# Kernel optimization log

Hardware: AMD Instinct MI355X
Metric: run time of the kernel (lower is better)

## Reference

```python
import math
import jax, jax.numpy as jnp
import numpy as np

B, K_LEN, Q_LEN = 16, 1024, 1024
E, N_HEAD, H = 1024, 8, 128

def setup_inputs() -> dict:
    key = jax.random.key(0)
    ks = jax.random.split(key, 7)
    k = jax.random.normal(ks[0], (B, K_LEN, E), dtype=jnp.float32)
    q = jax.random.normal(ks[1], (B, Q_LEN, E), dtype=jnp.float32)
    w_kx = jax.random.normal(ks[2], (N_HEAD, E, H), dtype=jnp.float32) * (1.0 / math.sqrt(E))
    w_qx = jax.random.normal(ks[3], (N_HEAD, E, H), dtype=jnp.float32) * (1.0 / math.sqrt(E))
    proj_w = jax.random.normal(ks[4], (E, N_HEAD * H), dtype=jnp.float32) * (1.0 / math.sqrt(N_HEAD * H))
    proj_b = jax.random.normal(ks[5], (E,), dtype=jnp.float32) * 0.01
    memory_len = jax.random.randint(ks[6], (B,), 0, K_LEN, dtype=jnp.int32)
    return {"k": k, "q": q, "w_kx": w_kx, "w_qx": w_qx, "proj_w": proj_w, "proj_b": proj_b, "memory_len": memory_len}

def reference(k, q, w_kx, w_qx, proj_w, proj_b, memory_len):
    n_head, embed_dim, hidden = w_kx.shape
    mb, k_len, _ = k.shape
    q_len = q.shape[1]
    # Faithful replication of torch repeat/view pairing:
    # row idx in [0, n_head*mb): data batch = idx % mb, weight head = idx % n_head
    idx = jnp.arange(n_head * mb)
    kx = jnp.einsum('nse,neh->nsh', k[idx % mb], w_kx[idx % n_head])   # [nB, k_len, H]
    qx = jnp.einsum('nse,neh->nsh', q[idx % mb], w_qx[idx % n_head])   # [nB, q_len, H]
    score = jnp.einsum('nqh,nkh->nqk', qx, kx) / math.sqrt(hidden)     # [nB, q_len, k_len]
    # 1D memory_len path: per-batch key-length mask, tiled over heads
    valid = jnp.arange(k_len)[None, :] < memory_len[:, None]           # [B, k_len]
    valid = jnp.tile(valid, (n_head, 1))[:, None, :]                   # [nB, 1, k_len]
    score = jnp.where(valid, score, jnp.float32(-10000.0))
    attn = jax.nn.softmax(score, axis=-1)
    out = jnp.einsum('nqk,nkh->nqh', attn, kx)                         # [nB, q_len, H]
    # torch.cat(torch.split(out, mb, 0), -1): chunk j -> feature block j
    out = out.reshape(n_head, mb, q_len, hidden).transpose(1, 2, 0, 3).reshape(mb, q_len, n_head * hidden)
    out = out @ proj_w.T + proj_b                                      # [B, q_len, E]
    return out, attn
```

## Files before the change

### kernel.cpp

```cpp
#include <hip/hip_runtime.h>
#include <hip/hip_bf16.h>

#define NBATCH 16
#define SEQ    1024
#define EDIM   1024
#define HDIM   128
#define RSQRT_H 0.08838834764831845f


typedef short s8b __attribute__((ext_vector_type(8)));
typedef float f32x4 __attribute__((ext_vector_type(4)));

__device__ __forceinline__ unsigned short bfr(float f) {
    unsigned u = __float_as_uint(f);
    u += 0x7fffu + ((u >> 16) & 1u);
    return (unsigned short)(u >> 16);
}

__device__ __forceinline__ f32x4 MFMA(s8b a, s8b b, f32x4 c) {
    return __builtin_amdgcn_mfma_f32_16x16x32_bf16(a, b, c, 0, 0, 0);
}

__global__ __launch_bounds__(256) void projx_mfma(const float* __restrict__ X,
                                                  const unsigned short* __restrict__ WT,
                                                  unsigned short* __restrict__ OUT) {
    const int b  = blockIdx.y;
    const int bm = blockIdx.x * 32;
    const int lane = threadIdx.x & 63, w = threadIdx.x >> 6;
    const int wn = w * 32;
    const int r = lane & 15, ko4 = lane >> 4, ko = ko4 * 8;

    const unsigned short* Bb = WT + (size_t)(b & 7) * 131072 + (size_t)(wn + r) * 1024 + ko;
    const float* Ab = X + (size_t)b * 1048576 + (size_t)(bm + r) * 1024 + ko;
    f32x4 acc[2][2] = {};

    for (int k = 0; k < 1024; k += 32) {
        s8b a0, a1;
        float4 u0 = *(const float4*)(Ab + k);
        float4 u1 = *(const float4*)(Ab + k + 4);
        a0[0]=(short)bfr(u0.x); a0[1]=(short)bfr(u0.y);
        a0[2]=(short)bfr(u0.z); a0[3]=(short)bfr(u0.w);
        a0[4]=(short)bfr(u1.x); a0[5]=(short)bfr(u1.y);
        a0[6]=(short)bfr(u1.z); a0[7]=(short)bfr(u1.w);
        float4 v0 = *(const float4*)(Ab + (size_t)16 * 1024 + k);
        float4 v1 = *(const float4*)(Ab + (size_t)16 * 1024 + k + 4);
        a1[0]=(short)bfr(v0.x); a1[1]=(short)bfr(v0.y);
        a1[2]=(short)bfr(v0.z); a1[3]=(short)bfr(v0.w);
        a1[4]=(short)bfr(v1.x); a1[5]=(short)bfr(v1.y);
        a1[6]=(short)bfr(v1.z); a1[7]=(short)bfr(v1.w);
        s8b b0 = *(const s8b*)(Bb + k);
        s8b b1 = *(const s8b*)(Bb + (size_t)16 * 1024 + k);
        acc[0][0] = MFMA(a0, b0, acc[0][0]);
        acc[0][1] = MFMA(a0, b1, acc[0][1]);
        acc[1][0] = MFMA(a1, b0, acc[1][0]);
        acc[1][1] = MFMA(a1, b1, acc[1][1]);
    }
#pragma unroll
    for (int i = 0; i < 2; ++i)
#pragma unroll
    for (int j = 0; j < 2; ++j) {
        const int row0 = bm + i * 16 + ko4 * 4;
        const int col  = wn + j * 16 + r;
#pragma unroll
        for (int jj = 0; jj < 4; ++jj)
            OUT[((size_t)b * SEQ + row0 + jj) * HDIM + col] = bfr(acc[i][j][jj]);
    }
}

__global__ __launch_bounds__(256) void projout_mfma(const float* __restrict__ Ap,
                                                    const unsigned short* __restrict__ Bp,
                                                    float* __restrict__ Cp,
                                                    const float* __restrict__ bias) {
    const int b  = blockIdx.z;
    const int bm = blockIdx.x * 64, bn = blockIdx.y * 64;
    const int lane = threadIdx.x & 63, w = threadIdx.x >> 6;
    const int wm = (w >> 1) * 32, wn = (w & 1) * 32;
    const int r = lane & 15, ko4 = lane >> 4, ko = ko4 * 8;

    const unsigned short* Bb = Bp + (size_t)(bn + wn + r) * HDIM + ko;
    const float* Ab = (const float*)Ap + (size_t)b * SEQ * HDIM
                      + (size_t)(bm + wm + r) * HDIM + ko;
    f32x4 acc[2][2] = {};
    for (int k = 0; k < HDIM; k += 32) {
        s8b a0, a1;
        float4 u0 = *(const float4*)(Ab + k);
        float4 u1 = *(const float4*)(Ab + k + 4);
        a0[0]=(short)bfr(u0.x); a0[1]=(short)bfr(u0.y);
        a0[2]=(short)bfr(u0.z); a0[3]=(short)bfr(u0.w);
        a0[4]=(short)bfr(u1.x); a0[5]=(short)bfr(u1.y);
        a0[6]=(short)bfr(u1.z); a0[7]=(short)bfr(u1.w);
        float4 v0 = *(const float4*)(Ab + (size_t)16 * HDIM + k);
        float4 v1 = *(const float4*)(Ab + (size_t)16 * HDIM + k + 4);
        a1[0]=(short)bfr(v0.x); a1[1]=(short)bfr(v0.y);
        a1[2]=(short)bfr(v0.z); a1[3]=(short)bfr(v0.w);
        a1[4]=(short)bfr(v1.x); a1[5]=(short)bfr(v1.y);
        a1[6]=(short)bfr(v1.z); a1[7]=(short)bfr(v1.w);
        s8b b0 = *(const s8b*)(Bb + k);
        s8b b1 = *(const s8b*)(Bb + (size_t)16 * HDIM + k);
        acc[0][0] = MFMA(a0, b0, acc[0][0]);
        acc[0][1] = MFMA(a0, b1, acc[0][1]);
        acc[1][0] = MFMA(a1, b0, acc[1][0]);
        acc[1][1] = MFMA(a1, b1, acc[1][1]);
    }
#pragma unroll
    for (int i = 0; i < 2; ++i)
#pragma unroll
    for (int j = 0; j < 2; ++j) {
        const int row0 = bm + wm + i * 16 + ko4 * 4;
        const int col  = bn + wn + j * 16 + r;
        const float bv = bias[col];
#pragma unroll
        for (int jj = 0; jj < 4; ++jj)
            Cp[(size_t)b * SEQ * EDIM + (size_t)(row0 + jj) * EDIM + col]
                = acc[i][j][jj] + bv;
    }
}

__global__ __launch_bounds__(256) void weff_kernel(const float* __restrict__ proj_w,
                                                   unsigned short* __restrict__ weffb) {
    int i = blockIdx.x * 256 + threadIdx.x;
    int e = i >> 7, h = i & 127;
    const float* p = proj_w + (size_t)e * (8 * HDIM) + h;
    float s = 0.f;
#pragma unroll
    for (int j = 0; j < 8; ++j) s += p[j * HDIM];
    weffb[i] = bfr(s);
}

__global__ __launch_bounds__(256) void wt_kernel(const float* __restrict__ src,
                                                 unsigned short* __restrict__ dst) {
    __shared__ unsigned short tile[32][40];
    const int hd = blockIdx.z, e0 = blockIdx.x * 32, h0 = blockIdx.y * 32;
    const int t = threadIdx.x, r = t >> 3, c = (t & 7) * 4;
    float4 v = *(const float4*)(src + ((size_t)hd * 1024 + e0 + r) * 128 + h0 + c);
    tile[r][c]     = bfr(v.x);
    tile[r][c + 1] = bfr(v.y);
    tile[r][c + 2] = bfr(v.z);
    tile[r][c + 3] = bfr(v.w);
    __syncthreads();
    ushort4 o;
    o.x = tile[c][r]; o.y = tile[c + 1][r]; o.z = tile[c + 2][r]; o.w = tile[c + 3][r];
    *(ushort4*)(dst + ((size_t)hd * 128 + h0 + r) * 1024 + e0 + c) = o;
}

__global__ __launch_bounds__(256) void kxt_kernel(const unsigned short* __restrict__ src,
                                                  unsigned short* __restrict__ dst) {
    __shared__ unsigned short tile[32][40];
    const int b = blockIdx.z, s0 = blockIdx.x * 32, h0 = blockIdx.y * 32;
    const int t = threadIdx.x, r = t >> 3, c = (t & 7) * 4;
    *(ushort4*)&tile[r][c] =
        *(const ushort4*)(src + ((size_t)b * 1024 + s0 + r) * 128 + h0 + c);
    __syncthreads();
    ushort4 o;
    o.x = tile[c][r]; o.y = tile[c + 1][r]; o.z = tile[c + 2][r]; o.w = tile[c + 3][r];
    *(ushort4*)(dst + ((size_t)b * 128 + h0 + r) * 1024 + s0 + c) = o;
}

__global__ __launch_bounds__(256) void fused_attn(
        const unsigned short* __restrict__ qxh, const unsigned short* __restrict__ kxh,
        const unsigned short* __restrict__ kxT, const int* __restrict__ mlen,
        float* __restrict__ attn0, float* __restrict__ outb) {
    __shared__ unsigned short Ph[16][1048];
    __shared__ float redm[4][16];
    __shared__ float redl[4][16];

    const int flat = blockIdx.y * 64 + blockIdx.x;
    const int work = (flat & 7) * 128 + (flat >> 3);
    const int b  = work >> 6;
    const int q0 = (work & 63) * 16;

    const int t = threadIdx.x, w = t >> 6, lane = t & 63;
    const int r = lane & 15, ko4 = lane >> 4, ko = ko4 * 8;
    const int ml = mlen[b];

    s8b aq[4];
#pragma unroll
    for (int ks = 0; ks < 4; ++ks)
        aq[ks] = *(const s8b*)(qxh + ((size_t)b * SEQ + q0 + r) * HDIM + ks * 32 + ko);

    f32x4 sacc[16];
#pragma unroll
    for (int i = 0; i < 16; ++i) {
        const int n0 = (w + 4 * i) * 16;
        f32x4 acc = {};
#pragma unroll
        for (int ks = 0; ks < 4; ++ks) {
            s8b bk = *(const s8b*)(kxh + ((size_t)b * SEQ + n0 + r) * HDIM + ks * 32 + ko);
            acc = MFMA(aq[ks], bk, acc);
        }
        sacc[i] = acc;
    }

    float pm[4] = {-3.0e38f, -3.0e38f, -3.0e38f, -3.0e38f};
#pragma unroll
    for (int i = 0; i < 16; ++i) {
        const int col = (w + 4 * i) * 16 + r;
#pragma unroll
        for (int jj = 0; jj < 4; ++jj) {
            float x = sacc[i][jj] * RSQRT_H;
            x = (col < ml) ? x : -10000.0f;
            sacc[i][jj] = x;
            pm[jj] = fmaxf(pm[jj], x);
        }
    }
#pragma unroll
    for (int d = 1; d < 16; d <<= 1)
#pragma unroll
        for (int jj = 0; jj < 4; ++jj) pm[jj] = fmaxf(pm[jj], __shfl_xor(pm[jj], d));
    if (r == 0) {
#pragma unroll
        for (int jj = 0; jj < 4; ++jj) redm[w][ko4 * 4 + jj] = pm[jj];
    }
    __syncthreads();
    float m[4];
#pragma unroll
    for (int jj = 0; jj < 4; ++jj) {
        const int row = ko4 * 4 + jj;
        m[jj] = fmaxf(fmaxf(redm[0][row], redm[1][row]),
                      fmaxf(redm[2][row], redm[3][row]));
    }
    float pl[4] = {0.f, 0.f, 0.f, 0.f};
#pragma unroll
    for (int i = 0; i < 16; ++i)
#pragma unroll
        for (int jj = 0; jj < 4; ++jj) {
            float e = __expf(sacc[i][jj] - m[jj]);
            sacc[i][jj] = e;
            pl[jj] += e;
        }
#pragma unroll
    for (int d = 1; d < 16; d <<= 1)
#pragma unroll
        for (int jj = 0; jj < 4; ++jj) pl[jj] += __shfl_xor(pl[jj], d);
    if (r == 0) {
#pragma unroll
        for (int jj = 0; jj < 4; ++jj) redl[w][ko4 * 4 + jj] = pl[jj];
    }
    __syncthreads();
    float li[4];
#pragma unroll
    for (int jj = 0; jj < 4; ++jj) {
        const int row = ko4 * 4 + jj;
        li[jj] = 1.0f / (redl[0][row] + redl[1][row] + redl[2][row] + redl[3][row]);
    }

    const size_t RB = (size_t)NBATCH * SEQ * SEQ;
    float* base0 = attn0 + (size_t)b * SEQ * SEQ;
    const bool wr2 = (b >= 7);
#pragma unroll
    for (int i = 0; i < 16; ++i) {
        const int n0 = (w + 4 * i) * 16;
#pragma unroll
        for (int jj = 0; jj < 4; ++jj) {
            const int row = ko4 * 4 + jj;
            const float y = sacc[i][jj] * li[jj];
            const size_t off = (size_t)(q0 + row) * SEQ + n0 + r;
            base0[off]          = y;
            base0[off + RB]     = y;
            base0[off + 3 * RB] = y;
            base0[off + 4 * RB] = y;
            base0[off + 5 * RB] = y;
            base0[off + 6 * RB] = y;
            base0[off + 7 * RB] = y;
            if (wr2) base0[off + 2 * RB] = y;
            Ph[row][n0 + r] = bfr(y);
        }
    }
    __syncthreads();

    f32x4 acc2[2] = {};
    for (int ks = 0; ks < 32; ++ks) {
        s8b pa = *(const s8b*)(&Ph[r][ks * 32 + ko]);
#pragma unroll
        for (int c = 0; c < 2; ++c) {
            const int n0 = (w * 2 + c) * 16;
            s8b bk = *(const s8b*)(kxT + ((size_t)b * HDIM + n0 + r) * SEQ + ks * 32 + ko);
            acc2[c] = MFMA(pa, bk, acc2[c]);
        }
    }
#pragma unroll
    for (int c = 0; c < 2; ++c) {
        const int n0 = (w * 2 + c) * 16;
#pragma unroll
        for (int jj = 0; jj < 4; ++jj)
            outb[((size_t)b * SEQ + q0 + ko4 * 4 + jj) * HDIM + n0 + r] = acc2[c][jj];
    }
}

__global__ __launch_bounds__(256) void fixup_kernel(const uint4* __restrict__ src,
                                                    uint4* __restrict__ dst) {
    size_t i = (size_t)blockIdx.x * 256 + threadIdx.x;
    dst[i] = src[i];
}

extern "C" void kernel_launch(void* const* d_in, const int* in_sizes, int n_in,
                              void* d_out, int out_size, void* d_ws, size_t ws_size,
                              hipStream_t stream) {
    const float* k      = (const float*)d_in[0];
    const float* q      = (const float*)d_in[1];
    const float* w_kx   = (const float*)d_in[2];
    const float* w_qx   = (const float*)d_in[3];
    const float* proj_w = (const float*)d_in[4];
    const float* proj_b = (const float*)d_in[5];
    const int*   mlen   = (const int*)d_in[6];

    float* out0  = (float*)d_out;
    float* attn0 = out0 + (size_t)NBATCH * SEQ * EDIM;
    const size_t BLK = (size_t)NBATCH * SEQ * SEQ;

    unsigned short* sc16 = (unsigned short*)(attn0 + 2 * BLK);
    unsigned short* wkT   = sc16;
    unsigned short* wqT   = wkT + 1048576;
    unsigned short* weffb = wqT + 1048576;
    unsigned short* qxh   = weffb + 131072;
    unsigned short* kxh   = qxh + 2097152;
    unsigned short* kxT   = kxh + 2097152;
    float*          outb  = (float*)(kxT + 2097152);

    weff_kernel<<<512, 256, 0, stream>>>(proj_w, weffb);
    wt_kernel<<<dim3(32, 4, 8), 256, 0, stream>>>(w_kx, wkT);
    wt_kernel<<<dim3(32, 4, 8), 256, 0, stream>>>(w_qx, wqT);

    projx_mfma<<<dim3(32, 16), 256, 0, stream>>>(k, wkT, kxh);
    projx_mfma<<<dim3(32, 16), 256, 0, stream>>>(q, wqT, qxh);

    kxt_kernel<<<dim3(32, 4, 16), 256, 0, stream>>>(kxh, kxT);

    fused_attn<<<dim3(64, 16), 256, 0, stream>>>(qxh, kxh, kxT, mlen, attn0, outb);

    projout_mfma<<<dim3(16, 16, 16), 256, 0, stream>>>(outb, weffb, out0, proj_b);

    fixup_kernel<<<7168, 256, 0, stream>>>((const uint4*)attn0,
                                           (uint4*)(attn0 + 2 * BLK));
}
```

Before: 311.4 us.

## Fuse output projection into attention epilogue and move scratch to workspace

The separate projout kernel is removed. Each attention block now rounds its PV result to bf16 in shared memory and multiplies it by the head-summed projection weight with MFMA, writing the final output plus bias directly. This drops the fp32 intermediate buffer round trip and one kernel launch. When the harness workspace is large enough, scratch buffers move there. The attention kernel then writes every attention replica itself, so the trailing fixup copy kernel is skipped. Launch bounds also request 4 blocks per CU. The risks are more register and shared-memory pressure, and a longer tail in the attention kernel.

```diff
diff --git a/kernel.cpp b/kernel.cpp
--- a/kernel.cpp
+++ b/kernel.cpp
@@ -67,55 +67,6 @@
     }
 }
 
-__global__ __launch_bounds__(256) void projout_mfma(const float* __restrict__ Ap,
-                                                    const unsigned short* __restrict__ Bp,
-                                                    float* __restrict__ Cp,
-                                                    const float* __restrict__ bias) {
-    const int b  = blockIdx.z;
-    const int bm = blockIdx.x * 64, bn = blockIdx.y * 64;
-    const int lane = threadIdx.x & 63, w = threadIdx.x >> 6;
-    const int wm = (w >> 1) * 32, wn = (w & 1) * 32;
-    const int r = lane & 15, ko4 = lane >> 4, ko = ko4 * 8;
-
-    const unsigned short* Bb = Bp + (size_t)(bn + wn + r) * HDIM + ko;
-    const float* Ab = (const float*)Ap + (size_t)b * SEQ * HDIM
-                      + (size_t)(bm + wm + r) * HDIM + ko;
-    f32x4 acc[2][2] = {};
-    for (int k = 0; k < HDIM; k += 32) {
-        s8b a0, a1;
-        float4 u0 = *(const float4*)(Ab + k);
-        float4 u1 = *(const float4*)(Ab + k + 4);
-        a0[0]=(short)bfr(u0.x); a0[1]=(short)bfr(u0.y);
-        a0[2]=(short)bfr(u0.z); a0[3]=(short)bfr(u0.w);
-        a0[4]=(short)bfr(u1.x); a0[5]=(short)bfr(u1.y);
-        a0[6]=(short)bfr(u1.z); a0[7]=(short)bfr(u1.w);
-        float4 v0 = *(const float4*)(Ab + (size_t)16 * HDIM + k);
-        float4 v1 = *(const float4*)(Ab + (size_t)16 * HDIM + k + 4);
-        a1[0]=(short)bfr(v0.x); a1[1]=(short)bfr(v0.y);
-        a1[2]=(short)bfr(v0.z); a1[3]=(short)bfr(v0.w);
-        a1[4]=(short)bfr(v1.x); a1[5]=(short)bfr(v1.y);
-        a1[6]=(short)bfr(v1.z); a1[7]=(short)bfr(v1.w);
-        s8b b0 = *(const s8b*)(Bb + k);
-        s8b b1 = *(const s8b*)(Bb + (size_t)16 * HDIM + k);
-        acc[0][0] = MFMA(a0, b0, acc[0][0]);
-        acc[0][1] = MFMA(a0, b1, acc[0][1]);
-        acc[1][0] = MFMA(a1, b0, acc[1][0]);
-        acc[1][1] = MFMA(a1, b1, acc[1][1]);
-    }
-#pragma unroll
-    for (int i = 0; i < 2; ++i)
-#pragma unroll
-    for (int j = 0; j < 2; ++j) {
-        const int row0 = bm + wm + i * 16 + ko4 * 4;
-        const int col  = bn + wn + j * 16 + r;
-        const float bv = bias[col];
-#pragma unroll
-        for (int jj = 0; jj < 4; ++jj)
-            Cp[(size_t)b * SEQ * EDIM + (size_t)(row0 + jj) * EDIM + col]
-                = acc[i][j][jj] + bv;
-    }
-}
-
 __global__ __launch_bounds__(256) void weff_kernel(const float* __restrict__ proj_w,
                                                    unsigned short* __restrict__ weffb) {
     int i = blockIdx.x * 256 + threadIdx.x;
@@ -156,11 +107,13 @@
     *(ushort4*)(dst + ((size_t)b * 128 + h0 + r) * 1024 + s0 + c) = o;
 }
 
-__global__ __launch_bounds__(256) void fused_attn(
+__global__ __launch_bounds__(256, 4) void fused_attn(
         const unsigned short* __restrict__ qxh, const unsigned short* __restrict__ kxh,
-        const unsigned short* __restrict__ kxT, const int* __restrict__ mlen,
-        float* __restrict__ attn0, float* __restrict__ outb) {
+        const unsigned short* __restrict__ kxT, const unsigned short* __restrict__ weffb,
+        const float* __restrict__ proj_b, const int* __restrict__ mlen,
+        float* __restrict__ attn0, float* __restrict__ out0, int wr_all) {
     __shared__ unsigned short Ph[16][1048];
+    __shared__ unsigned short PVa[16][132];
     __shared__ float redm[4][16];
     __shared__ float redl[4][16];
 
@@ -246,7 +199,7 @@
 
     const size_t RB = (size_t)NBATCH * SEQ * SEQ;
     float* base0 = attn0 + (size_t)b * SEQ * SEQ;
-    const bool wr2 = (b >= 7);
+    const bool wr2 = wr_all || (b >= 5);
 #pragma unroll
     for (int i = 0; i < 16; ++i) {
         const int n0 = (w + 4 * i) * 16;
@@ -283,7 +236,28 @@
         const int n0 = (w * 2 + c) * 16;
 #pragma unroll
         for (int jj = 0; jj < 4; ++jj)
-            outb[((size_t)b * SEQ + q0 + ko4 * 4 + jj) * HDIM + n0 + r] = acc2[c][jj];
+            PVa[ko4 * 4 + jj][n0 + r] = bfr(acc2[c][jj]);
+    }
+    __syncthreads();
+
+    s8b av[4];
+#pragma unroll
+    for (int ks = 0; ks < 4; ++ks)
+        av[ks] = *(const s8b*)(&PVa[r][ks * 32 + ko]);
+    float* ob = out0 + (size_t)b * SEQ * EDIM + (size_t)q0 * EDIM;
+#pragma unroll
+    for (int i = 0; i < 16; ++i) {
+        const int e0 = (w + 4 * i) * 16;
+        f32x4 acc = {};
+#pragma unroll
+        for (int ks = 0; ks < 4; ++ks) {
+            s8b bk = *(const s8b*)(weffb + (size_t)(e0 + r) * HDIM + ks * 32 + ko);
+            acc = MFMA(av[ks], bk, acc);
+        }
+        const float bv = proj_b[e0 + r];
+#pragma unroll
+        for (int jj = 0; jj < 4; ++jj)
+            ob[(size_t)(ko4 * 4 + jj) * EDIM + e0 + r] = acc[jj] + bv;
     }
 }
 
@@ -308,14 +282,18 @@
     float* attn0 = out0 + (size_t)NBATCH * SEQ * EDIM;
     const size_t BLK = (size_t)NBATCH * SEQ * SEQ;
 
-    unsigned short* sc16 = (unsigned short*)(attn0 + 2 * BLK);
+    const size_t SCRATCH_SHORTS = 1048576ull * 2 + 131072 + 2097152ull * 3;
+    const size_t NEED = SCRATCH_SHORTS * 2;
+    const int use_ws = (ws_size >= NEED) ? 1 : 0;
+
+    unsigned short* sc16 = use_ws ? (unsigned short*)d_ws
+                                  : (unsigned short*)(attn0 + 2 * BLK);
     unsigned short* wkT   = sc16;
     unsigned short* wqT   = wkT + 1048576;
     unsigned short* weffb = wqT + 1048576;
     unsigned short* qxh   = weffb + 131072;
     unsigned short* kxh   = qxh + 2097152;
     unsigned short* kxT   = kxh + 2097152;
-    float*          outb  = (float*)(kxT + 2097152);
 
     weff_kernel<<<512, 256, 0, stream>>>(proj_w, weffb);
     wt_kernel<<<dim3(32, 4, 8), 256, 0, stream>>>(w_kx, wkT);
@@ -326,10 +304,10 @@
 
     kxt_kernel<<<dim3(32, 4, 16), 256, 0, stream>>>(kxh, kxT);
 
-    fused_attn<<<dim3(64, 16), 256, 0, stream>>>(qxh, kxh, kxT, mlen, attn0, outb);
-
-    projout_mfma<<<dim3(16, 16, 16), 256, 0, stream>>>(outb, weffb, out0, proj_b);
-
-    fixup_kernel<<<7168, 256, 0, stream>>>((const uint4*)attn0,
-                                           (uint4*)(attn0 + 2 * BLK));
-}
+    fused_attn<<<dim3(64, 16), 256, 0, stream>>>(qxh, kxh, kxT, weffb, proj_b,
+                                                 mlen, attn0, out0, use_ws);
+
+    if (!use_ws)
+        fixup_kernel<<<5120, 256, 0, stream>>>((const uint4*)attn0,
+                                               (uint4*)(attn0 + 2 * BLK));
+}
```

Result: no change. 316.6 us (+1.7%).
